# Kernel optimization log

Hardware: AMD Instinct MI355X
Metric: run time of the kernel (lower is better)

## Reference

```python
import jax, jax.numpy as jnp
import numpy as np

SIGMA = 1.5
KSIZE = 15

def _log_kernel(sigma=SIGMA, k=KSIZE):
    ax = np.arange(k, dtype=np.float32) - k // 2
    xx, yy, zz = np.meshgrid(ax, ax, ax, indexing='ij')
    rr2 = xx**2 + yy**2 + zz**2
    g = np.exp(-rr2 / (2.0 * sigma**2))
    g = g / g.sum()
    log = (rr2 - 3.0 * sigma**2) / sigma**4 * g
    log = log - log.mean()
    return jnp.asarray(log.reshape(1, 1, k, k, k), dtype=jnp.float32)  # OIDHW

_KERNEL = _log_kernel()
_PAD = KSIZE // 2

def setup_inputs() -> dict:
    key = jax.random.key(0)
    k1, k2 = jax.random.split(key)
    shape = (4, 160, 160, 160)
    pred = jax.random.normal(k1, shape, dtype=jnp.float32)
    target = jax.random.normal(k2, shape, dtype=jnp.float32)
    return {"pred": pred, "target": target}

def _conv_log(x):
    # x: [B, D, H, W] -> [B, 1, D, H, W] conv with LoG kernel, 'same' padding
    x = x[:, None]  # NCDHW
    return jax.lax.conv_general_dilated(
        x, _KERNEL.astype(x.dtype),
        window_strides=(1, 1, 1),
        padding=[(_PAD, _PAD)] * 3,
        dimension_numbers=('NCDHW', 'OIDHW', 'NCDHW'))

def reference(pred, target):
    fp = _conv_log(pred)
    ft = _conv_log(target)
    return jnp.mean(jnp.abs(fp - ft))
```

## Files before the change

kernel.cpp:

```cpp
#include <hip/hip_runtime.h>
#include <hip/hip_fp16.h>
#include <math.h>

#define KS   15
#define RAD  7
#define L    160
#define VOL  (L*L*L)
#define NB   4
#define WTL  32
#define HALO (L + 2*RAD)
#define RPT  5
#define DT   40
#define NBLK (5*10*16)

typedef float fx2 __attribute__((ext_vector_type(2)));
typedef float fx4 __attribute__((ext_vector_type(4)));

struct Taps {
    float g[KS];
    float h[KS];
    float m;
    float scale;
};

__device__ __forceinline__ fx4 ld4z(const float* __restrict__ p, int w) {
    if (w >= 0 && w + 3 < L) return *reinterpret_cast<const fx4*>(p + w);
    fx4 r;
    r.x = (w     >= 0 && w     < L) ? p[w]     : 0.f;
    r.y = (w + 1 >= 0 && w + 1 < L) ? p[w + 1] : 0.f;
    r.z = (w + 2 >= 0 && w + 2 < L) ? p[w + 2] : 0.f;
    r.w = (w + 3 >= 0 && w + 3 < L) ? p[w + 3] : 0.f;
    return r;
}

__global__ __launch_bounds__(256) void k_wh(const float* __restrict__ pred,
                                            const float* __restrict__ tgt,
                                            __half2* __restrict__ PQ,
                                            __half* __restrict__ Rb,
                                            Taps tp) {
    __shared__ float   sA[HALO][WTL];
    __shared__ float   sB[HALO][WTL];
    __shared__ __half2 sC[HALO][WTL / 2];

    const int tid = threadIdx.x;
    const int wt  = blockIdx.x;
    const int wb  = wt * WTL;
    const int d   = blockIdx.y;
    const int n   = blockIdx.z;
    const size_t nbase = (size_t)n * VOL;
    const float* __restrict__ pro = pred + nbase + (size_t)d * L * L;
    const float* __restrict__ tro = tgt  + nbase + (size_t)d * L * L;
    const bool wedge = (wt == 0) || (wt == 4);

    for (int task = tid; task < HALO * 4; task += 256) {
        const int r  = task >> 2;
        const int j2 = task & 3;
        const int h  = r - RAD;
        if (h >= 0 && h < L) {
            const float* pr = pro + h * L;
            const float* tr = tro + h * L;
            const int w0 = wb + 8 * j2 - 8;
            float dv[24];
            if (!wedge) {
#pragma unroll
                for (int q = 0; q < 6; ++q) {
                    fx4 pv = *reinterpret_cast<const fx4*>(pr + w0 + 4 * q);
                    fx4 tv = *reinterpret_cast<const fx4*>(tr + w0 + 4 * q);
                    fx4 dd = pv - tv;
                    dv[4*q+0] = dd.x; dv[4*q+1] = dd.y;
                    dv[4*q+2] = dd.z; dv[4*q+3] = dd.w;
                }
            } else {
#pragma unroll
                for (int q = 0; q < 6; ++q) {
                    fx4 pv = ld4z(pr, w0 + 4 * q);
                    fx4 tv = ld4z(tr, w0 + 4 * q);
                    fx4 dd = pv - tv;
                    dv[4*q+0] = dd.x; dv[4*q+1] = dd.y;
                    dv[4*q+2] = dd.z; dv[4*q+3] = dd.w;
                }
            }
#pragma unroll
            for (int kp = 0; kp < 8; kp += 2) {
                fx2 mid = {dv[kp + 8], dv[kp + 9]};
                fx2 aa = tp.g[7] * mid;
                fx2 bb = tp.h[7] * mid;
                fx2 cc = mid;
#pragma unroll
                for (int u = 0; u < 7; ++u) {
                    fx2 sl = {dv[kp + 1 + u],  dv[kp + 2 + u]};
                    fx2 sr = {dv[kp + 15 - u], dv[kp + 16 - u]};
                    fx2 s  = sl + sr;
                    aa += tp.g[u] * s;
                    bb += tp.h[u] * s;
                    cc += s;
                }
                *reinterpret_cast<fx2*>(&sA[r][8*j2 + kp]) = aa;
                *reinterpret_cast<fx2*>(&sB[r][8*j2 + kp]) = bb;
                sC[r][(8*j2 + kp) >> 1] = __floats2half2_rn(cc.x, cc.y);
            }
        } else {
#pragma unroll
            for (int kp = 0; kp < 8; kp += 2) {
                fx2 z = {0.f, 0.f};
                *reinterpret_cast<fx2*>(&sA[r][8*j2 + kp]) = z;
                *reinterpret_cast<fx2*>(&sB[r][8*j2 + kp]) = z;
                sC[r][(8*j2 + kp) >> 1] = __floats2half2_rn(0.f, 0.f);
            }
        }
    }
    __syncthreads();

    {
        const int wg = tid & 7;
        const int ty = tid >> 3;
        fx2 p[RPT][2], q[RPT][2], rb[RPT][2];
#pragma unroll
        for (int k = 0; k < RPT; ++k) {
            p[k][0] = 0.f; p[k][1] = 0.f;
            q[k][0] = 0.f; q[k][1] = 0.f;
            rb[k][0] = 0.f; rb[k][1] = 0.f;
        }
#pragma unroll
        for (int jr = 0; jr < RPT + 2 * RAD; ++jr) {
            const int srow = RPT * ty + jr;
            fx4 va4 = *reinterpret_cast<const fx4*>(&sA[srow][4*wg]);
            fx4 vb4 = *reinterpret_cast<const fx4*>(&sB[srow][4*wg]);
            fx2 va_lo = __builtin_shufflevector(va4, va4, 0, 1);
            fx2 va_hi = __builtin_shufflevector(va4, va4, 2, 3);
            fx2 vb_lo = __builtin_shufflevector(vb4, vb4, 0, 1);
            fx2 vb_hi = __builtin_shufflevector(vb4, vb4, 2, 3);
            const __half2* cp = &sC[srow][2*wg];
            float2 c0 = __half22float2(cp[0]);
            float2 c1 = __half22float2(cp[1]);
            fx2 vc_lo = {c0.x, c0.y};
            fx2 vc_hi = {c1.x, c1.y};
#pragma unroll
            for (int k = 0; k < RPT; ++k) {
                const int t = jr - k;
                if (t >= 0 && t < KS) {
                    p[k][0]  += tp.g[t] * va_lo;
                    p[k][1]  += tp.g[t] * va_hi;
                    q[k][0]  += tp.h[t] * va_lo + tp.g[t] * vb_lo;
                    q[k][1]  += tp.h[t] * va_hi + tp.g[t] * vb_hi;
                    rb[k][0] += vc_lo;
                    rb[k][1] += vc_hi;
                }
            }
        }
#pragma unroll
        for (int k = 0; k < RPT; ++k) {
            const int h = RPT * ty + k;
            const size_t o = nbase + ((size_t)h * L + d) * L + wb + 4*wg;
            __half2 pq[4];
            pq[0] = __floats2half2_rn(p[k][0].x, q[k][0].x);
            pq[1] = __floats2half2_rn(p[k][0].y, q[k][0].y);
            pq[2] = __floats2half2_rn(p[k][1].x, q[k][1].x);
            pq[3] = __floats2half2_rn(p[k][1].y, q[k][1].y);
            *reinterpret_cast<int4*>(&PQ[o]) = *reinterpret_cast<int4*>(pq);
            __half2 rr[2];
            rr[0] = __floats2half2_rn(rb[k][0].x, rb[k][0].y);
            rr[1] = __floats2half2_rn(rb[k][1].x, rb[k][1].y);
            *reinterpret_cast<int2*>(&Rb[o]) = *reinterpret_cast<int2*>(rr);
        }
    }
}

__global__ __launch_bounds__(512) void k_d(const __half2* __restrict__ PQ,
                                           const __half* __restrict__ R,
                                           float* __restrict__ partial,
                                           Taps tp) {
    const int tx = threadIdx.x;
    const int ty = threadIdx.y;
    const int w  = blockIdx.x * 32 + tx;
    const int h  = blockIdx.y * 16 + ty;
    const int gz = blockIdx.z;
    const int n  = gz >> 2;
    const int dc = gz & 3;
    const int d0 = dc * DT;

    const size_t base = (size_t)n * VOL + ((size_t)h * L) * L + w;
    const __half2* PQp = PQ + base;
    const __half*  Rp  = R  + base;

    float rp[KS], rq[KS], rc[KS];
    float box = 0.f;

#pragma unroll
    for (int i = 0; i < KS - 1; ++i) {
        int s = d0 - RAD + i;
        bool ok = (s >= 0);
        int off = s * L;
        float2 pq = make_float2(0.f, 0.f);
        float vc = 0.f;
        if (ok) {
            pq = __half22float2(PQp[off]);
            vc = __half2float(Rp[off]);
        }
        rp[i] = pq.x; rq[i] = pq.y; rc[i] = vc;
        box += vc;
    }

    float acc = 0.f;
#pragma unroll
    for (int k = 0; k < DT; ++k) {
        int s = d0 + RAD + k;
        bool ok = (s < L);
        int off = s * L;
        float2 pq = make_float2(0.f, 0.f);
        float vc = 0.f;
        if (ok) {
            pq = __half22float2(PQp[off]);
            vc = __half2float(Rp[off]);
        }
        const int ri = (KS - 1 + k) % KS;
        rp[ri] = pq.x; rq[ri] = pq.y; rc[ri] = vc;
        box += vc;

        float f = 0.f;
#pragma unroll
        for (int t = 0; t < KS; ++t) {
            const int ii = (k + t) % KS;
            f += tp.h[t] * rp[ii] + tp.g[t] * rq[ii];
        }
        f -= tp.m * box;
        acc += fabsf(f);

        box -= rc[k % KS];
    }
    acc *= tp.scale;

#pragma unroll
    for (int off = 32; off > 0; off >>= 1) acc += __shfl_down(acc, off);

    __shared__ float wsum[8];
    const int tid  = ty * 32 + tx;
    const int lane = tid & 63;
    const int wid  = tid >> 6;
    if (lane == 0) wsum[wid] = acc;
    __syncthreads();
    if (wid == 0) {
        float v = (lane < 8) ? wsum[lane] : 0.f;
#pragma unroll
        for (int off = 4; off > 0; off >>= 1) v += __shfl_down(v, off);
        if (lane == 0) {
            const int bid = (gz * gridDim.y + blockIdx.y) * gridDim.x + blockIdx.x;
            partial[bid] = v;
        }
    }
}

__global__ __launch_bounds__(1024) void k_reduce(const float* __restrict__ partial,
                                                 float* __restrict__ out) {
    float v = 0.f;
    for (int i = threadIdx.x; i < NBLK; i += 1024) v += partial[i];
#pragma unroll
    for (int off = 32; off > 0; off >>= 1) v += __shfl_down(v, off);

    __shared__ float wsum[16];
    const int lane = threadIdx.x & 63;
    const int wid  = threadIdx.x >> 6;
    if (lane == 0) wsum[wid] = v;
    __syncthreads();
    if (wid == 0) {
        float s = (lane < 16) ? wsum[lane] : 0.f;
#pragma unroll
        for (int off = 8; off > 0; off >>= 1) s += __shfl_down(s, off);
        if (lane == 0) out[0] = s;
    }
}

extern "C" void kernel_launch(void* const* d_in, const int* in_sizes, int n_in,
                              void* d_out, int out_size, void* d_ws, size_t ws_size,
                              hipStream_t stream) {
    const float* pred = (const float*)d_in[0];
    const float* tgt  = (const float*)d_in[1];
    float* out = (float*)d_out;

    Taps tp;
    const double sigma = 1.5;
    double g1[KS], S = 0.0;
    for (int i = 0; i < KS; ++i) {
        double x = (double)(i - RAD);
        g1[i] = exp(-x * x / (2.0 * sigma * sigma));
        S += g1[i];
    }
    double sumH = 0.0;
    for (int i = 0; i < KS; ++i) {
        double x = (double)(i - RAD);
        double G = g1[i] / S;
        double H = (x * x - sigma * sigma) / (sigma * sigma * sigma * sigma) * G;
        tp.g[i] = (float)G;
        tp.h[i] = (float)H;
        sumH += H;
    }
    tp.m     = (float)(3.0 * sumH / (double)(KS * KS * KS));
    tp.scale = 1.0f / ((float)NB * (float)VOL);

    char* wsb = (char*)d_ws;
    __half2* PQ      = (__half2*)wsb;
    __half*  Rb      = (__half*)(wsb + (size_t)NB * VOL * 4);
    float*   partial = (float*)(wsb + (size_t)NB * VOL * 6);

    k_wh<<<dim3(5, L, NB), dim3(256), 0, stream>>>(pred, tgt, PQ, Rb, tp);
    k_d<<<dim3(5, 10, NB * 4), dim3(32, 16), 0, stream>>>(PQ, Rb, partial, tp);
    k_reduce<<<1, 1024, 0, stream>>>(partial, out);
}
```

Baseline: 131.1 us.

## Split k_wh into H tiles of 80 rows and narrow per-thread width to two

The first-pass kernel now tiles the H dimension into two halves per block, doubling the grid, and each thread handles 2 columns instead of 4, with the shared-memory row stride padded to 34. This shrinks the LDS footprint per block and raises block count, aiming for better occupancy and fewer bank conflicts. The cost is extra halo rows loaded twice (14 of 94 per tile) and narrower stores to global memory.

```diff
diff --git a/kernel.cpp b/kernel.cpp
--- a/kernel.cpp
+++ b/kernel.cpp
@@ -8,7 +8,9 @@
 #define VOL  (L*L*L)
 #define NB   4
 #define WTL  32
-#define HALO (L + 2*RAD)
+#define HTL  80
+#define HALO (HTL + 2*RAD)
+#define LDA  34
 #define RPT  5
 #define DT   40
 #define NBLK (5*10*16)
@@ -38,13 +40,15 @@
                                             __half2* __restrict__ PQ,
                                             __half* __restrict__ Rb,
                                             Taps tp) {
-    __shared__ float   sA[HALO][WTL];
-    __shared__ float   sB[HALO][WTL];
-    __shared__ __half2 sC[HALO][WTL / 2];
+    __shared__ float   sA[HALO][LDA];
+    __shared__ float   sB[HALO][LDA];
+    __shared__ __half2 sC[HALO][LDA / 2];
 
     const int tid = threadIdx.x;
-    const int wt  = blockIdx.x;
+    const int wt  = blockIdx.x >> 1;
+    const int ht  = blockIdx.x & 1;
     const int wb  = wt * WTL;
+    const int h0  = ht * HTL;
     const int d   = blockIdx.y;
     const int n   = blockIdx.z;
     const size_t nbase = (size_t)n * VOL;
@@ -55,7 +59,7 @@
     for (int task = tid; task < HALO * 4; task += 256) {
         const int r  = task >> 2;
         const int j2 = task & 3;
-        const int h  = r - RAD;
+        const int h  = h0 - RAD + r;
         if (h >= 0 && h < L) {
             const float* pr = pro + h * L;
             const float* tr = tro + h * L;
@@ -112,56 +116,38 @@
     __syncthreads();
 
     {
-        const int wg = tid & 7;
-        const int ty = tid >> 3;
-        fx2 p[RPT][2], q[RPT][2], rb[RPT][2];
-#pragma unroll
-        for (int k = 0; k < RPT; ++k) {
-            p[k][0] = 0.f; p[k][1] = 0.f;
-            q[k][0] = 0.f; q[k][1] = 0.f;
-            rb[k][0] = 0.f; rb[k][1] = 0.f;
-        }
+        const int wg = tid & 15;
+        const int ty = tid >> 4;
+        fx2 p[RPT], q[RPT], rb[RPT];
+#pragma unroll
+        for (int k = 0; k < RPT; ++k) { p[k] = 0.f; q[k] = 0.f; rb[k] = 0.f; }
 #pragma unroll
         for (int jr = 0; jr < RPT + 2 * RAD; ++jr) {
             const int srow = RPT * ty + jr;
-            fx4 va4 = *reinterpret_cast<const fx4*>(&sA[srow][4*wg]);
-            fx4 vb4 = *reinterpret_cast<const fx4*>(&sB[srow][4*wg]);
-            fx2 va_lo = __builtin_shufflevector(va4, va4, 0, 1);
-            fx2 va_hi = __builtin_shufflevector(va4, va4, 2, 3);
-            fx2 vb_lo = __builtin_shufflevector(vb4, vb4, 0, 1);
-            fx2 vb_hi = __builtin_shufflevector(vb4, vb4, 2, 3);
-            const __half2* cp = &sC[srow][2*wg];
-            float2 c0 = __half22float2(cp[0]);
-            float2 c1 = __half22float2(cp[1]);
-            fx2 vc_lo = {c0.x, c0.y};
-            fx2 vc_hi = {c1.x, c1.y};
+            fx2 va = *reinterpret_cast<const fx2*>(&sA[srow][2*wg]);
+            fx2 vb = *reinterpret_cast<const fx2*>(&sB[srow][2*wg]);
+            float2 cf = __half22float2(sC[srow][wg]);
+            fx2 vc = {cf.x, cf.y};
 #pragma unroll
             for (int k = 0; k < RPT; ++k) {
                 const int t = jr - k;
                 if (t >= 0 && t < KS) {
-                    p[k][0]  += tp.g[t] * va_lo;
-                    p[k][1]  += tp.g[t] * va_hi;
-                    q[k][0]  += tp.h[t] * va_lo + tp.g[t] * vb_lo;
-                    q[k][1]  += tp.h[t] * va_hi + tp.g[t] * vb_hi;
-                    rb[k][0] += vc_lo;
-                    rb[k][1] += vc_hi;
+                    p[k]  += tp.g[t] * va;
+                    q[k]  += tp.h[t] * va + tp.g[t] * vb;
+                    rb[k] += vc;
                 }
             }
         }
 #pragma unroll
         for (int k = 0; k < RPT; ++k) {
-            const int h = RPT * ty + k;
-            const size_t o = nbase + ((size_t)h * L + d) * L + wb + 4*wg;
-            __half2 pq[4];
-            pq[0] = __floats2half2_rn(p[k][0].x, q[k][0].x);
-            pq[1] = __floats2half2_rn(p[k][0].y, q[k][0].y);
-            pq[2] = __floats2half2_rn(p[k][1].x, q[k][1].x);
-            pq[3] = __floats2half2_rn(p[k][1].y, q[k][1].y);
-            *reinterpret_cast<int4*>(&PQ[o]) = *reinterpret_cast<int4*>(pq);
-            __half2 rr[2];
-            rr[0] = __floats2half2_rn(rb[k][0].x, rb[k][0].y);
-            rr[1] = __floats2half2_rn(rb[k][1].x, rb[k][1].y);
-            *reinterpret_cast<int2*>(&Rb[o]) = *reinterpret_cast<int2*>(rr);
+            const int h = h0 + RPT * ty + k;
+            const size_t o = nbase + ((size_t)h * L + d) * L + wb + 2*wg;
+            __half2 pq[2];
+            pq[0] = __floats2half2_rn(p[k].x, q[k].x);
+            pq[1] = __floats2half2_rn(p[k].y, q[k].y);
+            *reinterpret_cast<int2*>(&PQ[o]) = *reinterpret_cast<int2*>(pq);
+            __half2 rr = __floats2half2_rn(rb[k].x, rb[k].y);
+            *reinterpret_cast<__half2*>(&Rb[o]) = rr;
         }
     }
 }
@@ -302,7 +288,7 @@
     __half*  Rb      = (__half*)(wsb + (size_t)NB * VOL * 4);
     float*   partial = (float*)(wsb + (size_t)NB * VOL * 6);
 
-    k_wh<<<dim3(5, L, NB), dim3(256), 0, stream>>>(pred, tgt, PQ, Rb, tp);
+    k_wh<<<dim3(10, L, NB), dim3(256), 0, stream>>>(pred, tgt, PQ, Rb, tp);
     k_d<<<dim3(5, 10, NB * 4), dim3(32, 16), 0, stream>>>(PQ, Rb, partial, tp);
     k_reduce<<<1, 1024, 0, stream>>>(partial, out);
 }
```

After: 128.1 us. 2.3% less time.
